# Performance work log

Measured on AMD Instinct MI355X. Metric: run time of the kernel, lower is better.

## Reference

```python
import jax, jax.numpy as jnp
import numpy as np

N_NODES = 20000   # original graph nodes
E_G = 200000      # original graph edges = line-graph nodes
E_LG = 2000000    # line-graph edges
D_IN = 64
D_H = 128


def setup_inputs() -> dict:
    key = jax.random.key(0)
    ks = jax.random.split(key, 9)
    x = jax.random.normal(ks[0], (N_NODES, D_IN), dtype=jnp.float32)
    g_edge_index = jax.random.randint(ks[1], (2, E_G), 0, N_NODES)
    lg_edge_index = jax.random.randint(ks[2], (2, E_LG), 0, E_G)
    s = 0.05
    W0 = jax.random.normal(ks[3], (2 * D_IN, D_H), dtype=jnp.float32) * s
    b0 = jnp.zeros((D_H,), dtype=jnp.float32)
    W1 = jax.random.normal(ks[4], (D_H, D_H), dtype=jnp.float32) * s
    b1 = jnp.zeros((D_H,), dtype=jnp.float32)
    Wl = jax.random.normal(ks[5], (D_H, 1), dtype=jnp.float32) * s
    bl = jnp.zeros((1,), dtype=jnp.float32)
    return {"x": x, "g_edge_index": g_edge_index, "lg_edge_index": lg_edge_index,
            "index01": 0, "W0": W0, "b0": b0, "W1": W1, "b1": b1, "Wl": Wl, "bl": bl}


def gcn_conv(h, edge_index, W, b, n):
    # PyG GCNConv: add self-loops, symmetric deg^{-1/2} normalization,
    # linear transform then gather-scale-scatter aggregation, then bias.
    loop = jnp.arange(n)
    row = jnp.concatenate([edge_index[0], loop])  # source j
    col = jnp.concatenate([edge_index[1], loop])  # target i
    deg = jax.ops.segment_sum(jnp.ones(row.shape, h.dtype), col, num_segments=n)
    dinv = jnp.where(deg > 0, jax.lax.rsqrt(deg), 0.0)
    norm = dinv[row] * dinv[col]                   # [E+n]
    hw = h @ W                                     # [n, D_out]
    msg = hw[row] * norm[:, None]                  # gather + scale
    out = jax.ops.segment_sum(msg, col, num_segments=n)  # scatter-add
    return out + b


def reference(x, g_edge_index, lg_edge_index, index01, W0, b0, W1, b1, Wl, bl):
    # to_line_graph_features: concat endpoint features per original edge
    h = jnp.concatenate([x[g_edge_index[0]], x[g_edge_index[1]]], axis=-1)  # [E_G, 2*D_IN]
    n = h.shape[0]
    h = jax.nn.relu(gcn_conv(h, lg_edge_index, W0, b0, n))
    h = jax.nn.relu(gcn_conv(h, lg_edge_index, W1, b1, n))
    sel = h[index01][None, :]                      # [1, D_H]
    return jax.nn.sigmoid(sel @ Wl + bl)           # [1, 1]
```

## Files before the change

kernel.cpp:

```cpp
#include <hip/hip_runtime.h>
#include <math.h>

#define MAX_L1 512
#define MAX_S2 (MAX_L1 + 8)
#define MAX_L2 4096
#define MAX_S3 (MAX_L2 + MAX_S2 + 8)
#define SCAN_B 1024
#define HW0_B 64
#define LDSE 1024

enum { CNT_L1 = 0, CNT_S2 = 1, CNT_L2 = 2, CNT_S3 = 3, CNT_TICKET = 4 };

__device__ __forceinline__ void insert_s3(int n, unsigned* bits3, int* cnt,
                                          int* s3_list, int* slot) {
  unsigned m = 1u << (n & 31);
  if (!(atomicOr(&bits3[n >> 5], m) & m)) {
    int p = atomicAdd(&cnt[CNT_S3], 1);
    if (p < MAX_S3) { s3_list[p] = n; slot[n] = p; }
  }
}

__device__ __forceinline__ void insert_s2(int n, unsigned* bits2, int* cnt,
                                          int* s2_list, int* s2pos,
                                          unsigned* bits3, int* s3_list,
                                          int* slot) {
  unsigned m = 1u << (n & 31);
  if (!(atomicOr(&bits2[n >> 5], m) & m)) {
    int p = atomicAdd(&cnt[CNT_S2], 1);
    if (p < MAX_S2) { s2_list[p] = n; s2pos[n] = p; }
  }
  insert_s3(n, bits3, cnt, s3_list, slot);
}

__global__ void __launch_bounds__(256) k_scan1(
    const int* __restrict__ lg, int e_lg, const int* __restrict__ pidx,
    int* __restrict__ cnt, unsigned* __restrict__ bits2,
    unsigned* __restrict__ bits3, int* __restrict__ list1,
    int* __restrict__ s2_list, int* __restrict__ s2pos,
    int* __restrict__ s3_list, int* __restrict__ slot) {
  const int idx0 = pidx[0];
  const int gtid = blockIdx.x * blockDim.x + threadIdx.x;
  const int gstride = gridDim.x * blockDim.x;
  if (gtid == 0) insert_s2(idx0, bits2, cnt, s2_list, s2pos, bits3, s3_list, slot);
  const int* __restrict__ col = lg + e_lg;
  const int n4 = ((((uintptr_t)col) & 15) == 0) ? (e_lg >> 2) : 0;
  const int4* __restrict__ col4 = (const int4*)col;
  for (int i = gtid; i < n4; i += gstride) {
    int4 v = col4[i];
    int cc[4] = {v.x, v.y, v.z, v.w};
#pragma unroll
    for (int k = 0; k < 4; ++k) {
      if (cc[k] == idx0) {
        int r = lg[i * 4 + k];
        int p = atomicAdd(&cnt[CNT_L1], 1);
        if (p < MAX_L1) list1[p] = r;
        insert_s2(r, bits2, cnt, s2_list, s2pos, bits3, s3_list, slot);
      }
    }
  }
  for (int e = n4 * 4 + gtid; e < e_lg; e += gstride) {
    if (col[e] == idx0) {
      int r = lg[e];
      int p = atomicAdd(&cnt[CNT_L1], 1);
      if (p < MAX_L1) list1[p] = r;
      insert_s2(r, bits2, cnt, s2_list, s2pos, bits3, s3_list, slot);
    }
  }
}

__global__ void __launch_bounds__(256) k_scan2(
    const int* __restrict__ lg, int e_lg, int* __restrict__ cnt,
    const unsigned* __restrict__ bits2, unsigned* __restrict__ bits3,
    int2* __restrict__ list2, int* __restrict__ s3_list,
    int* __restrict__ slot) {
  const int gtid = blockIdx.x * blockDim.x + threadIdx.x;
  const int gstride = gridDim.x * blockDim.x;
  const int* __restrict__ col = lg + e_lg;
  const int n4 = ((((uintptr_t)col) & 15) == 0) ? (e_lg >> 2) : 0;
  const int4* __restrict__ col4 = (const int4*)col;
  for (int i = gtid; i < n4; i += gstride) {
    int4 v = col4[i];
    int cc[4] = {v.x, v.y, v.z, v.w};
#pragma unroll
    for (int k = 0; k < 4; ++k) {
      int c = cc[k];
      if ((bits2[c >> 5] >> (c & 31)) & 1u) {
        int r = lg[i * 4 + k];
        int p = atomicAdd(&cnt[CNT_L2], 1);
        if (p < MAX_L2) list2[p] = make_int2(r, c);
        insert_s3(r, bits3, cnt, s3_list, slot);
      }
    }
  }
  for (int e = n4 * 4 + gtid; e < e_lg; e += gstride) {
    int c = col[e];
    if ((bits2[c >> 5] >> (c & 31)) & 1u) {
      int r = lg[e];
      int p = atomicAdd(&cnt[CNT_L2], 1);
      if (p < MAX_L2) list2[p] = make_int2(r, c);
      insert_s3(r, bits3, cnt, s3_list, slot);
    }
  }
}

__global__ void __launch_bounds__(256) k_deg_hw0(
    const int* __restrict__ lg, int e_lg, const float* __restrict__ x,
    const int* __restrict__ g, int e_g, const float* __restrict__ W0,
    const int* __restrict__ cnt, const unsigned* __restrict__ bits3,
    const int* __restrict__ slot, int* __restrict__ degc,
    const int* __restrict__ s3_list, float* __restrict__ hw0) {
  const int tid = threadIdx.x;
  if (blockIdx.x < SCAN_B) {
    const int gtid = blockIdx.x * blockDim.x + tid;
    const int gstride = SCAN_B * blockDim.x;
    const int* __restrict__ col = lg + e_lg;
    const int n4 = ((((uintptr_t)col) & 15) == 0) ? (e_lg >> 2) : 0;
    const int4* __restrict__ col4 = (const int4*)col;
    for (int i = gtid; i < n4; i += gstride) {
      int4 v = col4[i];
      int cc[4] = {v.x, v.y, v.z, v.w};
#pragma unroll
      for (int k = 0; k < 4; ++k) {
        int c = cc[k];
        if ((bits3[c >> 5] >> (c & 31)) & 1u) atomicAdd(&degc[slot[c]], 1);
      }
    }
    for (int e = n4 * 4 + gtid; e < e_lg; e += gstride) {
      int c = col[e];
      if ((bits3[c >> 5] >> (c & 31)) & 1u) atomicAdd(&degc[slot[c]], 1);
    }
  } else {
    int ns3 = min(cnt[CNT_S3], MAX_S3);
    int hb = (blockIdx.x - SCAN_B) * 2 + (tid >> 7);
    int t = tid & 127;
    for (int b = hb; b < ns3; b += HW0_B * 2) {
      int node = s3_list[b];
      int src = g[node];
      int dst = g[e_g + node];
      float acc = 0.f;
#pragma unroll 8
      for (int k = 0; k < 64; ++k) acc += x[src * 64 + k] * W0[k * 128 + t];
#pragma unroll 8
      for (int k = 0; k < 64; ++k) acc += x[dst * 64 + k] * W0[(64 + k) * 128 + t];
      hw0[b * 128 + t] = acc;
    }
  }
}

__global__ void __launch_bounds__(256) k_h1_hw1_final(
    int* __restrict__ cnt, const int* __restrict__ pidx,
    const int* __restrict__ s2_list, const int* __restrict__ s2pos,
    const int* __restrict__ slot, const int* __restrict__ degc,
    const int* __restrict__ list1, const int2* __restrict__ list2,
    const float* __restrict__ hw0, const float* __restrict__ b0,
    const float* __restrict__ W1, const float* __restrict__ b1,
    const float* __restrict__ Wl, const float* __restrict__ bl,
    float* __restrict__ hw1, float* __restrict__ out) {
  int ns2 = min(cnt[CNT_S2], MAX_S2);
  if ((int)blockIdx.x >= ns2) return;
  const int tid = threadIdx.x;
  int t = tid & 127;
  int grp = tid >> 7;
  __shared__ int2 eLDS[LDSE];
  __shared__ float part[2][128];
  __shared__ float h1s[128];

  int j = s2_list[blockIdx.x];
  int n2 = min(cnt[CNT_L2], MAX_L2);
  int n2l = min(n2, LDSE);
  for (int i = tid; i < n2l; i += 256) eLDS[i] = list2[i];
  __syncthreads();

  float dj = rsqrtf((float)degc[slot[j]] + 1.0f);
  float acc = (grp == 0) ? hw0[slot[j] * 128 + t] * dj * dj + b0[t] : 0.f;
  for (int i = grp; i < n2; i += 2) {
    int2 e = (i < LDSE) ? eLDS[i] : list2[i];
    if (e.y == j) {
      float dr = rsqrtf((float)degc[slot[e.x]] + 1.0f);
      acc += hw0[slot[e.x] * 128 + t] * (dr * dj);
    }
  }
  part[grp][t] = acc;
  __syncthreads();
  if (grp == 0) h1s[t] = fmaxf(part[0][t] + part[1][t], 0.f);
  __syncthreads();
  float a2 = 0.f;
  int k0 = grp * 64;
#pragma unroll 8
  for (int k = 0; k < 64; ++k) a2 += h1s[k0 + k] * W1[(k0 + k) * 128 + t];
  part[grp][t] = a2;
  __syncthreads();
  if (grp == 0) hw1[blockIdx.x * 128 + t] = part[0][t] + part[1][t];

  __syncthreads();
  __threadfence();
  __shared__ int is_last;
  if (tid == 0) is_last = (atomicAdd(&cnt[CNT_TICKET], 1) == ns2 - 1);
  __syncthreads();
  if (!is_last) return;
  __threadfence();

  int idx0 = pidx[0];
  float d0 = rsqrtf((float)degc[slot[idx0]] + 1.0f);
  float facc = (grp == 0) ? hw1[s2pos[idx0] * 128 + t] * d0 * d0 : 0.f;
  int n1 = min(cnt[CNT_L1], MAX_L1);
  for (int i = grp; i < n1; i += 2) {
    int r = list1[i];
    float dr = rsqrtf((float)degc[slot[r]] + 1.0f);
    facc += hw1[s2pos[r] * 128 + t] * (dr * d0);
  }
  part[grp][t] = facc;
  __syncthreads();
  if (grp == 0) {
    float h2 = fmaxf(part[0][t] + part[1][t] + b1[t], 0.f);
    h1s[t] = h2 * Wl[t];
  }
  __syncthreads();
  if (grp == 0) {
    for (int s = 64; s > 0; s >>= 1) {
      if (t < s) h1s[t] += h1s[t + s];
      __syncthreads();
    }
    if (t == 0) out[0] = 1.f / (1.f + expf(-(h1s[0] + bl[0])));
  }
}

extern "C" void kernel_launch(void* const* d_in, const int* in_sizes, int n_in,
                              void* d_out, int out_size, void* d_ws, size_t ws_size,
                              hipStream_t stream) {
  const float* x  = (const float*)d_in[0];
  const int* g    = (const int*)d_in[1];
  const int* lg   = (const int*)d_in[2];
  const int* pidx = (const int*)d_in[3];
  const float* W0 = (const float*)d_in[4];
  const float* b0 = (const float*)d_in[5];
  const float* W1 = (const float*)d_in[6];
  const float* b1 = (const float*)d_in[7];
  const float* Wl = (const float*)d_in[8];
  const float* bl = (const float*)d_in[9];
  float* out = (float*)d_out;

  int e_g = in_sizes[1] / 2;
  int e_lg = in_sizes[2] / 2;

  char* ws = (char*)d_ws;
  size_t off = 0;
  auto take = [&](size_t bytes) {
    size_t cur = off;
    off = (off + bytes + 15) & ~(size_t)15;
    return cur;
  };
  const size_t nbits_words = ((size_t)e_g + 31) / 32;
  int* cnt        = (int*)(ws + take(16 * 4));
  unsigned* bits2 = (unsigned*)(ws + take(nbits_words * 4));
  unsigned* bits3 = (unsigned*)(ws + take(nbits_words * 4));
  int* degc       = (int*)(ws + take((size_t)MAX_S3 * 4));
  size_t zero_bytes = off;
  int* list1      = (int*)(ws + take(MAX_L1 * 4));
  int* s2_list    = (int*)(ws + take(MAX_S2 * 4));
  int* s2pos      = (int*)(ws + take((size_t)e_g * 4));
  int2* list2     = (int2*)(ws + take((size_t)MAX_L2 * 8));
  int* s3_list    = (int*)(ws + take((size_t)MAX_S3 * 4));
  int* slot       = (int*)(ws + take((size_t)e_g * 4));
  float* hw0      = (float*)(ws + take((size_t)MAX_S3 * 128 * 4));
  float* hw1      = (float*)(ws + take((size_t)MAX_S2 * 128 * 4));
  (void)ws_size;

  hipMemsetAsync(d_ws, 0, zero_bytes, stream);

  k_scan1<<<SCAN_B, 256, 0, stream>>>(lg, e_lg, pidx, cnt, bits2, bits3,
                                      list1, s2_list, s2pos, s3_list, slot);
  k_scan2<<<SCAN_B, 256, 0, stream>>>(lg, e_lg, cnt, bits2, bits3, list2,
                                      s3_list, slot);
  k_deg_hw0<<<SCAN_B + HW0_B, 256, 0, stream>>>(
      lg, e_lg, x, g, e_g, W0, cnt, bits3, slot, degc, s3_list, hw0);
  k_h1_hw1_final<<<MAX_S2, 256, 0, stream>>>(
      cnt, pidx, s2_list, s2pos, slot, degc, list1, list2, hw0, b0, W1, b1,
      Wl, bl, hw1, out);
}
```

Baseline: 154.2 us.

## Fuse four pipeline kernels into one cooperative kernel with global barriers

Merges the scan1, scan2, degree/hw0, and h1/hw1/final kernels into a single cooperative launch with 1024 blocks. Phases are separated by hand-written atomic-counter grid barriers, and the final readout runs on block 0 instead of using the last-block ticket. This is meant to remove the launch gaps and tail drains between the four dependent kernels. In exchange the degree-count phase gets fewer scan blocks (960 instead of 1024), and it relies on all 1024 blocks being co-resident, which a cooperative launch is meant to guarantee.

Result: slower. 550.3 us (+256.8%).

```diff
diff --git a/kernel.cpp b/kernel.cpp
--- a/kernel.cpp
+++ b/kernel.cpp
@@ -1,15 +1,31 @@
 #include <hip/hip_runtime.h>
 #include <math.h>
+
 
 #define MAX_L1 512
 #define MAX_S2 (MAX_L1 + 8)
 #define MAX_L2 4096
 #define MAX_S3 (MAX_L2 + MAX_S2 + 8)
-#define SCAN_B 1024
+#define GRID_B 1024
 #define HW0_B 64
+#define SCAN_C (GRID_B - HW0_B)
 #define LDSE 1024
 
-enum { CNT_L1 = 0, CNT_S2 = 1, CNT_L2 = 2, CNT_S3 = 3, CNT_TICKET = 4 };
+enum { CNT_L1 = 0, CNT_S2 = 1, CNT_L2 = 2, CNT_S3 = 3,
+       BAR_A = 8, BAR_B = 9, BAR_C = 10, BAR_D = 11 };
+
+__device__ __forceinline__ void gbar(int* ctr, int expected) {
+  __syncthreads();
+  if (threadIdx.x == 0) {
+    __threadfence();
+    atomicAdd(ctr, 1);
+    while (__hip_atomic_load(ctr, __ATOMIC_RELAXED,
+                             __HIP_MEMORY_SCOPE_AGENT) < expected)
+      __builtin_amdgcn_s_sleep(4);
+    __threadfence();
+  }
+  __syncthreads();
+}
 
 __device__ __forceinline__ void insert_s3(int n, unsigned* bits3, int* cnt,
                                           int* s3_list, int* slot) {
@@ -32,19 +48,34 @@
   insert_s3(n, bits3, cnt, s3_list, slot);
 }
 
-__global__ void __launch_bounds__(256) k_scan1(
-    const int* __restrict__ lg, int e_lg, const int* __restrict__ pidx,
-    int* __restrict__ cnt, unsigned* __restrict__ bits2,
-    unsigned* __restrict__ bits3, int* __restrict__ list1,
-    int* __restrict__ s2_list, int* __restrict__ s2pos,
-    int* __restrict__ s3_list, int* __restrict__ slot) {
+__global__ void __launch_bounds__(256)
+fused_gnn(const float* __restrict__ x, const int* __restrict__ g,
+          const int* __restrict__ lg, const int* __restrict__ pidx,
+          const float* __restrict__ W0, const float* __restrict__ b0,
+          const float* __restrict__ W1, const float* __restrict__ b1,
+          const float* __restrict__ Wl, const float* __restrict__ bl,
+          float* __restrict__ out,
+          int* __restrict__ cnt, unsigned* __restrict__ bits2,
+          unsigned* __restrict__ bits3, int* __restrict__ degc,
+          int* __restrict__ list1, int* __restrict__ s2_list,
+          int* __restrict__ s2pos, int2* __restrict__ list2,
+          int* __restrict__ s3_list, int* __restrict__ slot,
+          float* __restrict__ hw0, float* __restrict__ hw1,
+          int e_g, int e_lg) {
+  const int tid = threadIdx.x;
+  const int gtid = blockIdx.x * blockDim.x + tid;
+  const int gstride = GRID_B * 256;
   const int idx0 = pidx[0];
-  const int gtid = blockIdx.x * blockDim.x + threadIdx.x;
-  const int gstride = gridDim.x * blockDim.x;
-  if (gtid == 0) insert_s2(idx0, bits2, cnt, s2_list, s2pos, bits3, s3_list, slot);
   const int* __restrict__ col = lg + e_lg;
   const int n4 = ((((uintptr_t)col) & 15) == 0) ? (e_lg >> 2) : 0;
   const int4* __restrict__ col4 = (const int4*)col;
+
+  __shared__ int2 eLDS[LDSE];
+  __shared__ float part[2][128];
+  __shared__ float h1s[128];
+
+  if (gtid == 0)
+    insert_s2(idx0, bits2, cnt, s2_list, s2pos, bits3, s3_list, slot);
   for (int i = gtid; i < n4; i += gstride) {
     int4 v = col4[i];
     int cc[4] = {v.x, v.y, v.z, v.w};
@@ -66,18 +97,8 @@
       insert_s2(r, bits2, cnt, s2_list, s2pos, bits3, s3_list, slot);
     }
   }
-}
-
-__global__ void __launch_bounds__(256) k_scan2(
-    const int* __restrict__ lg, int e_lg, int* __restrict__ cnt,
-    const unsigned* __restrict__ bits2, unsigned* __restrict__ bits3,
-    int2* __restrict__ list2, int* __restrict__ s3_list,
-    int* __restrict__ slot) {
-  const int gtid = blockIdx.x * blockDim.x + threadIdx.x;
-  const int gstride = gridDim.x * blockDim.x;
-  const int* __restrict__ col = lg + e_lg;
-  const int n4 = ((((uintptr_t)col) & 15) == 0) ? (e_lg >> 2) : 0;
-  const int4* __restrict__ col4 = (const int4*)col;
+  gbar(&cnt[BAR_A], GRID_B);
+
   for (int i = gtid; i < n4; i += gstride) {
     int4 v = col4[i];
     int cc[4] = {v.x, v.y, v.z, v.w};
@@ -101,22 +122,12 @@
       insert_s3(r, bits3, cnt, s3_list, slot);
     }
   }
-}
-
-__global__ void __launch_bounds__(256) k_deg_hw0(
-    const int* __restrict__ lg, int e_lg, const float* __restrict__ x,
-    const int* __restrict__ g, int e_g, const float* __restrict__ W0,
-    const int* __restrict__ cnt, const unsigned* __restrict__ bits3,
-    const int* __restrict__ slot, int* __restrict__ degc,
-    const int* __restrict__ s3_list, float* __restrict__ hw0) {
-  const int tid = threadIdx.x;
-  if (blockIdx.x < SCAN_B) {
-    const int gtid = blockIdx.x * blockDim.x + tid;
-    const int gstride = SCAN_B * blockDim.x;
-    const int* __restrict__ col = lg + e_lg;
-    const int n4 = ((((uintptr_t)col) & 15) == 0) ? (e_lg >> 2) : 0;
-    const int4* __restrict__ col4 = (const int4*)col;
-    for (int i = gtid; i < n4; i += gstride) {
+  gbar(&cnt[BAR_B], GRID_B);
+
+  if (blockIdx.x < SCAN_C) {
+    const int sgtid = blockIdx.x * 256 + tid;
+    const int sstride = SCAN_C * 256;
+    for (int i = sgtid; i < n4; i += sstride) {
       int4 v = col4[i];
       int cc[4] = {v.x, v.y, v.z, v.w};
 #pragma unroll
@@ -125,13 +136,13 @@
         if ((bits3[c >> 5] >> (c & 31)) & 1u) atomicAdd(&degc[slot[c]], 1);
       }
     }
-    for (int e = n4 * 4 + gtid; e < e_lg; e += gstride) {
+    for (int e = n4 * 4 + sgtid; e < e_lg; e += sstride) {
       int c = col[e];
       if ((bits3[c >> 5] >> (c & 31)) & 1u) atomicAdd(&degc[slot[c]], 1);
     }
   } else {
     int ns3 = min(cnt[CNT_S3], MAX_S3);
-    int hb = (blockIdx.x - SCAN_B) * 2 + (tid >> 7);
+    int hb = (blockIdx.x - SCAN_C) * 2 + (tid >> 7);
     int t = tid & 127;
     for (int b = hb; b < ns3; b += HW0_B * 2) {
       int node = s3_list[b];
@@ -145,83 +156,67 @@
       hw0[b * 128 + t] = acc;
     }
   }
-}
-
-__global__ void __launch_bounds__(256) k_h1_hw1_final(
-    int* __restrict__ cnt, const int* __restrict__ pidx,
-    const int* __restrict__ s2_list, const int* __restrict__ s2pos,
-    const int* __restrict__ slot, const int* __restrict__ degc,
-    const int* __restrict__ list1, const int2* __restrict__ list2,
-    const float* __restrict__ hw0, const float* __restrict__ b0,
-    const float* __restrict__ W1, const float* __restrict__ b1,
-    const float* __restrict__ Wl, const float* __restrict__ bl,
-    float* __restrict__ hw1, float* __restrict__ out) {
-  int ns2 = min(cnt[CNT_S2], MAX_S2);
-  if ((int)blockIdx.x >= ns2) return;
-  const int tid = threadIdx.x;
-  int t = tid & 127;
-  int grp = tid >> 7;
-  __shared__ int2 eLDS[LDSE];
-  __shared__ float part[2][128];
-  __shared__ float h1s[128];
-
-  int j = s2_list[blockIdx.x];
-  int n2 = min(cnt[CNT_L2], MAX_L2);
-  int n2l = min(n2, LDSE);
-  for (int i = tid; i < n2l; i += 256) eLDS[i] = list2[i];
-  __syncthreads();
-
-  float dj = rsqrtf((float)degc[slot[j]] + 1.0f);
-  float acc = (grp == 0) ? hw0[slot[j] * 128 + t] * dj * dj + b0[t] : 0.f;
-  for (int i = grp; i < n2; i += 2) {
-    int2 e = (i < LDSE) ? eLDS[i] : list2[i];
-    if (e.y == j) {
-      float dr = rsqrtf((float)degc[slot[e.x]] + 1.0f);
-      acc += hw0[slot[e.x] * 128 + t] * (dr * dj);
-    }
-  }
-  part[grp][t] = acc;
-  __syncthreads();
-  if (grp == 0) h1s[t] = fmaxf(part[0][t] + part[1][t], 0.f);
-  __syncthreads();
-  float a2 = 0.f;
-  int k0 = grp * 64;
+  gbar(&cnt[BAR_C], GRID_B);
+
+  {
+    int ns2 = min(cnt[CNT_S2], MAX_S2);
+    int n2 = min(cnt[CNT_L2], MAX_L2);
+    if ((int)blockIdx.x < ns2) {
+      int t = tid & 127;
+      int grp = tid >> 7;
+      int j = s2_list[blockIdx.x];
+      int n2l = min(n2, LDSE);
+      for (int i = tid; i < n2l; i += 256) eLDS[i] = list2[i];
+      __syncthreads();
+      float dj = rsqrtf((float)degc[slot[j]] + 1.0f);
+      float acc = (grp == 0) ? hw0[slot[j] * 128 + t] * dj * dj + b0[t] : 0.f;
+      for (int i = grp; i < n2; i += 2) {
+        int2 e = (i < LDSE) ? eLDS[i] : list2[i];
+        if (e.y == j) {
+          float dr = rsqrtf((float)degc[slot[e.x]] + 1.0f);
+          acc += hw0[slot[e.x] * 128 + t] * (dr * dj);
+        }
+      }
+      part[grp][t] = acc;
+      __syncthreads();
+      if (grp == 0) h1s[t] = fmaxf(part[0][t] + part[1][t], 0.f);
+      __syncthreads();
+      float a2 = 0.f;
+      int k0 = grp * 64;
 #pragma unroll 8
-  for (int k = 0; k < 64; ++k) a2 += h1s[k0 + k] * W1[(k0 + k) * 128 + t];
-  part[grp][t] = a2;
-  __syncthreads();
-  if (grp == 0) hw1[blockIdx.x * 128 + t] = part[0][t] + part[1][t];
-
-  __syncthreads();
-  __threadfence();
-  __shared__ int is_last;
-  if (tid == 0) is_last = (atomicAdd(&cnt[CNT_TICKET], 1) == ns2 - 1);
-  __syncthreads();
-  if (!is_last) return;
-  __threadfence();
-
-  int idx0 = pidx[0];
-  float d0 = rsqrtf((float)degc[slot[idx0]] + 1.0f);
-  float facc = (grp == 0) ? hw1[s2pos[idx0] * 128 + t] * d0 * d0 : 0.f;
-  int n1 = min(cnt[CNT_L1], MAX_L1);
-  for (int i = grp; i < n1; i += 2) {
-    int r = list1[i];
-    float dr = rsqrtf((float)degc[slot[r]] + 1.0f);
-    facc += hw1[s2pos[r] * 128 + t] * (dr * d0);
-  }
-  part[grp][t] = facc;
-  __syncthreads();
-  if (grp == 0) {
-    float h2 = fmaxf(part[0][t] + part[1][t] + b1[t], 0.f);
-    h1s[t] = h2 * Wl[t];
-  }
-  __syncthreads();
-  if (grp == 0) {
-    for (int s = 64; s > 0; s >>= 1) {
-      if (t < s) h1s[t] += h1s[t + s];
-      __syncthreads();
-    }
-    if (t == 0) out[0] = 1.f / (1.f + expf(-(h1s[0] + bl[0])));
+      for (int k = 0; k < 64; ++k) a2 += h1s[k0 + k] * W1[(k0 + k) * 128 + t];
+      part[grp][t] = a2;
+      __syncthreads();
+      if (grp == 0) hw1[blockIdx.x * 128 + t] = part[0][t] + part[1][t];
+    }
+  }
+  gbar(&cnt[BAR_D], GRID_B);
+
+  if (blockIdx.x == 0) {
+    int t = tid & 127;
+    int grp = tid >> 7;
+    float d0 = rsqrtf((float)degc[slot[idx0]] + 1.0f);
+    float facc = (grp == 0) ? hw1[s2pos[idx0] * 128 + t] * d0 * d0 : 0.f;
+    int n1 = min(cnt[CNT_L1], MAX_L1);
+    for (int i = grp; i < n1; i += 2) {
+      int r = list1[i];
+      float dr = rsqrtf((float)degc[slot[r]] + 1.0f);
+      facc += hw1[s2pos[r] * 128 + t] * (dr * d0);
+    }
+    part[grp][t] = facc;
+    __syncthreads();
+    if (grp == 0) {
+      float h2 = fmaxf(part[0][t] + part[1][t] + b1[t], 0.f);
+      h1s[t] = h2 * Wl[t];
+    }
+    __syncthreads();
+    if (grp == 0) {
+      for (int s = 64; s > 0; s >>= 1) {
+        if (t < s) h1s[t] += h1s[t + s];
+        __syncthreads();
+      }
+      if (t == 0) out[0] = 1.f / (1.f + expf(-(h1s[0] + bl[0])));
+    }
   }
 }
 
@@ -268,13 +263,14 @@
 
   hipMemsetAsync(d_ws, 0, zero_bytes, stream);
 
-  k_scan1<<<SCAN_B, 256, 0, stream>>>(lg, e_lg, pidx, cnt, bits2, bits3,
-                                      list1, s2_list, s2pos, s3_list, slot);
-  k_scan2<<<SCAN_B, 256, 0, stream>>>(lg, e_lg, cnt, bits2, bits3, list2,
-                                      s3_list, slot);
-  k_deg_hw0<<<SCAN_B + HW0_B, 256, 0, stream>>>(
-      lg, e_lg, x, g, e_g, W0, cnt, bits3, slot, degc, s3_list, hw0);
-  k_h1_hw1_final<<<MAX_S2, 256, 0, stream>>>(
-      cnt, pidx, s2_list, s2pos, slot, degc, list1, list2, hw0, b0, W1, b1,
-      Wl, bl, hw1, out);
-}
+  void* kargs[] = {
+      (void*)&x,   (void*)&g,     (void*)&lg,    (void*)&pidx,
+      (void*)&W0,  (void*)&b0,    (void*)&W1,    (void*)&b1,
+      (void*)&Wl,  (void*)&bl,    (void*)&out,
+      (void*)&cnt, (void*)&bits2, (void*)&bits3, (void*)&degc,
+      (void*)&list1, (void*)&s2_list, (void*)&s2pos, (void*)&list2,
+      (void*)&s3_list, (void*)&slot, (void*)&hw0, (void*)&hw1,
+      (void*)&e_g, (void*)&e_lg};
+  hipLaunchCooperativeKernel((const void*)fused_gnn, dim3(GRID_B), dim3(256),
+                             kargs, 0, stream);
+}
```
